# Kernel optimization log

Hardware: AMD Instinct MI355X
Metric: run time of the kernel (lower is better)

## Reference

```python
import jax, jax.numpy as jnp
import numpy as np

B, S, D = 4, 2048, 1024

def setup_inputs() -> dict:
    key = jax.random.key(0)
    ks = jax.random.split(key, 7)
    s = 1.0 / np.sqrt(D)
    return {
        "x":  jax.random.normal(ks[0], (B, S, D), dtype=jnp.float32),
        "Wq": jax.random.uniform(ks[1], (D, D), jnp.float32, -s, s),
        "bq": jax.random.uniform(ks[2], (D,),  jnp.float32, -s, s),
        "Wk": jax.random.uniform(ks[3], (D, D), jnp.float32, -s, s),
        "bk": jax.random.uniform(ks[4], (D,),  jnp.float32, -s, s),
        "Wv": jax.random.uniform(ks[5], (D, D), jnp.float32, -s, s),
        "bv": jax.random.uniform(ks[6], (D,),  jnp.float32, -s, s),
    }

def reference(x, Wq, bq, Wk, bk, Wv, bv):
    # Q/K/V projections: [B,S,D]
    Q = jnp.einsum('bsd,de->bse', x, Wq) + bq
    K = jnp.einsum('bsd,de->bse', x, Wk) + bk
    V = jnp.einsum('bsd,de->bse', x, Wv) + bv
    scale = 1.0 / jnp.sqrt(jnp.asarray(K.shape[-1], K.dtype))
    scores = jnp.einsum('bqd,bkd->bqk', Q, K) * scale  # [B,S,S]
    weights = jax.nn.softmax(scores, axis=-1)
    return jnp.einsum('bqk,bkd->bqd', weights, V)
```

## Files before the change

kernel.cpp:

```cpp
#include <hip/hip_runtime.h>

typedef __attribute__((ext_vector_type(4))) float f32x4;
typedef __attribute__((ext_vector_type(8))) short bf16x8;

__device__ __forceinline__ float bf2f(unsigned short u) {
  union { unsigned int i; float f; } x; x.i = ((unsigned int)u) << 16; return x.f;
}
__device__ __forceinline__ unsigned short f2bf(float f) {
  union { float f; unsigned int i; } x; x.f = f;
  unsigned int r = (x.i + 0x7FFFu + ((x.i >> 16) & 1u)) >> 16;
  return (unsigned short)r;
}

#define BARX __builtin_amdgcn_s_barrier()
#define LGK0 asm volatile("s_waitcnt lgkmcnt(0)" ::: "memory")
#define GLD(gsrc, ldsoff)                                                        \
  __builtin_amdgcn_global_load_lds(                                              \
      (const __attribute__((address_space(1))) void*)(gsrc),                     \
      (__attribute__((address_space(3))) void*)&lds[ldsoff], 16, 0, 0)

__global__ __launch_bounds__(256) void cvt_f2b(const float* __restrict__ src,
                                               unsigned short* __restrict__ dst, long n4) {
  long i = (long)blockIdx.x * 256 + threadIdx.x;
  long stride = (long)gridDim.x * 256;
  for (; i < n4; i += stride) {
    float4 v = *(const float4*)&src[i * 4];
    ushort4 o;
    o.x = f2bf(v.x); o.y = f2bf(v.y); o.z = f2bf(v.z); o.w = f2bf(v.w);
    *(ushort4*)&dst[i * 4] = o;
  }
}

__global__ __launch_bounds__(256) void transpose_f2b(const float* __restrict__ src,
                                                     unsigned short* __restrict__ dst,
                                                     int rows, int cols) {
  __shared__ float t[32][33];
  int bx = blockIdx.x * 32, by = blockIdx.y * 32;
  int tx = threadIdx.x, ty = threadIdx.y;
#pragma unroll
  for (int k = 0; k < 4; ++k)
    t[ty + 8 * k][tx] = src[(long)(by + ty + 8 * k) * cols + bx + tx];
  __syncthreads();
#pragma unroll
  for (int k = 0; k < 4; ++k)
    dst[(long)(bx + ty + 8 * k) * rows + by + tx] = f2bf(t[tx][ty + 8 * k]);
}

__global__ __launch_bounds__(256) void transpose_v(const unsigned short* __restrict__ src,
                                                   unsigned short* __restrict__ dst) {
  __shared__ unsigned short t[32][33];
  const long sb = (long)blockIdx.z * 2048 * 3072;
  const long db = (long)blockIdx.z * 1024 * 2048;
  int bx = blockIdx.x * 32, by = blockIdx.y * 32;
  int tx = threadIdx.x, ty = threadIdx.y;
#pragma unroll
  for (int k = 0; k < 4; ++k)
    t[ty + 8 * k][tx] = src[sb + (long)(by + ty + 8 * k) * 3072 + bx + tx];
  __syncthreads();
#pragma unroll
  for (int k = 0; k < 4; ++k)
    dst[db + (long)(bx + ty + 8 * k) * 2048 + by + tx] = t[tx][ty + 8 * k];
}

template <int MODE>
__global__ __launch_bounds__(512, 2) void gemm2p(const unsigned short* __restrict__ Ap,
                                                 const unsigned short* __restrict__ Bp,
                                                 void* __restrict__ Cv,
                                                 const float* __restrict__ q_,
                                                 const float* __restrict__ k_,
                                                 const float* __restrict__ v_,
                                                 const float* __restrict__ invden,
                                                 int Kd, int lda, int ldb, int ldc, float scale,
                                                 long sA, long sB, long sC) {
  __shared__ unsigned short lds[73728];
  const int bz = blockIdx.z;
  Ap += (long)bz * sA; Bp += (long)bz * sB;
  const int tid = threadIdx.x;
  const int m0 = blockIdx.x * 128, n0 = blockIdx.y * 256;
  const int lane = tid & 63, wave = tid >> 6;
  const int wm = wave >> 2, wn = wave & 3;
  const int rr = tid >> 3;
  const int cSrc = ((tid & 7) ^ (rr & 7)) << 3;
  const int lc = lane & 15, lr = lane >> 4;
  const int x0 = (lc & 4) << 3;
  const int x1 = 32 ^ x0;
  const int klo = (lr << 3) ^ ((lc & 3) << 3);
  const int aoff = (wm * 64 + lc) * 64 + klo;
  const int boff = 8192 + (wn * 64 + lc) * 64 + klo;
  const int NT = Kd >> 6;

  const unsigned short* pA0 = Ap + (long)(m0 + rr) * lda + cSrc;
  const unsigned short* pA1 = pA0 + (long)64 * lda;
  const unsigned short* pB0 = Bp + (long)(n0 + rr) * ldb + cSrc;
  const unsigned short* pB1 = pB0 + (long)64 * ldb;
  const unsigned short* pB2 = pB0 + (long)128 * ldb;
  const unsigned short* pB3 = pB0 + (long)192 * ldb;
  const int dA0 = tid * 8, dA1 = 4096 + tid * 8;
  const int dB0 = 8192 + tid * 8, dB1 = 12288 + tid * 8;
  const int dB2 = 16384 + tid * 8, dB3 = 20480 + tid * 8;
#define STAGE6(so)                                                                \
  { GLD(pB0, (so) + dB0); GLD(pB1, (so) + dB1); GLD(pA0, (so) + dA0);             \
    GLD(pB2, (so) + dB2); GLD(pB3, (so) + dB3); GLD(pA1, (so) + dA1); }
#define ADV { pA0 += 64; pA1 += 64; pB0 += 64; pB1 += 64; pB2 += 64; pB3 += 64; }

  f32x4 acc[4][4] = {};

  STAGE6(0); ADV;
  STAGE6(24576); ADV;
  asm volatile("s_waitcnt vmcnt(6)" ::: "memory");
  BARX;

  int cur = 0;
  for (int t = 0; t < NT; ++t) {
    const int stg = (cur >= 1) ? cur - 1 : 2;
    const unsigned short* Lp = &lds[cur * 24576];
    const int so = stg * 24576;
    const bool pf = (t + 2 < NT);
    bf16x8 a0[2][2], a1[2][2], bb[2][2][2];
#pragma unroll
    for (int nh = 0; nh < 2; ++nh)
#pragma unroll
      for (int ni = 0; ni < 2; ++ni) {
        bb[nh][ni][0] = *(const bf16x8*)&Lp[boff + nh * 2048 + ni * 1024 + x0];
        bb[nh][ni][1] = *(const bf16x8*)&Lp[boff + nh * 2048 + ni * 1024 + x1];
      }
#pragma unroll
    for (int mi = 0; mi < 2; ++mi) {
      a0[mi][0] = *(const bf16x8*)&Lp[aoff + mi * 1024 + x0];
      a0[mi][1] = *(const bf16x8*)&Lp[aoff + mi * 1024 + x1];
    }
    if (pf) { GLD(pB0, so + dB0); GLD(pB1, so + dB1); GLD(pA0, so + dA0); }
    BARX; LGK0;
    __builtin_amdgcn_s_setprio(1);
#pragma unroll
    for (int mi = 0; mi < 2; ++mi)
#pragma unroll
      for (int nh = 0; nh < 2; ++nh)
#pragma unroll
        for (int ni = 0; ni < 2; ++ni)
#pragma unroll
          for (int x = 0; x < 2; ++x)
            acc[mi][nh * 2 + ni] = __builtin_amdgcn_mfma_f32_16x16x32_bf16(
                a0[mi][x], bb[nh][ni][x], acc[mi][nh * 2 + ni], 0, 0, 0);
    __builtin_amdgcn_s_setprio(0);
    BARX;
#pragma unroll
    for (int mi = 0; mi < 2; ++mi) {
      a1[mi][0] = *(const bf16x8*)&Lp[aoff + 2048 + mi * 1024 + x0];
      a1[mi][1] = *(const bf16x8*)&Lp[aoff + 2048 + mi * 1024 + x1];
    }
    if (pf) { GLD(pB2, so + dB2); GLD(pB3, so + dB3); GLD(pA1, so + dA1); }
    BARX; LGK0;
    __builtin_amdgcn_s_setprio(1);
#pragma unroll
    for (int mi = 0; mi < 2; ++mi)
#pragma unroll
      for (int nh = 0; nh < 2; ++nh)
#pragma unroll
        for (int ni = 0; ni < 2; ++ni)
#pragma unroll
          for (int x = 0; x < 2; ++x)
            acc[2 + mi][nh * 2 + ni] = __builtin_amdgcn_mfma_f32_16x16x32_bf16(
                a1[mi][x], bb[nh][ni][x], acc[2 + mi][nh * 2 + ni], 0, 0, 0);
    __builtin_amdgcn_s_setprio(0);
    if (pf) { asm volatile("s_waitcnt vmcnt(6)" ::: "memory"); }
    else    { asm volatile("s_waitcnt vmcnt(0)" ::: "memory"); }
    BARX;
    cur = (cur == 2) ? 0 : cur + 1;
    ADV;
  }
#undef STAGE6
#undef ADV

  const int r0 = m0 + wm * 64 + lr * 4;
  const int c0 = n0 + wn * 64 + lc;
  if (MODE == 2) {
    float* O = (float*)Cv + (long)bz * sC;
    const float* idn = invden + (long)bz * 2048;
#pragma unroll
    for (int j = 0; j < 4; ++j)
#pragma unroll
      for (int r = 0; r < 4; ++r) {
        const int row = r0 + j * 16 + r;
        const float iv = idn[row];
#pragma unroll
        for (int nh = 0; nh < 2; ++nh)
#pragma unroll
          for (int ni = 0; ni < 2; ++ni)
            O[(long)row * ldc + (c0 + nh * 32 + ni * 16)] = acc[j][nh * 2 + ni][r] * iv;
      }
  } else {
    unsigned short* C = (unsigned short*)Cv + (long)bz * sC;
#pragma unroll
    for (int nh = 0; nh < 2; ++nh)
#pragma unroll
      for (int ni = 0; ni < 2; ++ni) {
        const int col = c0 + nh * 32 + ni * 16;
        float bv = 0.0f;
        if (MODE == 0)
          bv = (col < 1024) ? q_[col] : ((col < 2048) ? k_[col - 1024] : v_[col - 2048]);
#pragma unroll
        for (int j = 0; j < 4; ++j)
#pragma unroll
          for (int r = 0; r < 4; ++r) {
            float val = acc[j][nh * 2 + ni][r];
            val = (MODE == 0) ? (val + bv) : __expf(val * scale);
            C[(long)(r0 + j * 16 + r) * ldc + col] = f2bf(val);
          }
      }
  }
}

__global__ __launch_bounds__(256) void rowsum_inv(const unsigned short* __restrict__ E,
                                                  float* __restrict__ invden) {
  const long row = blockIdx.x;
  const unsigned short* p = E + row * 2048;
  const int tid = threadIdx.x;
  const int lane = tid & 63, wave = tid >> 6;
  ushort4 h0 = *(const ushort4*)&p[tid * 8];
  ushort4 h1 = *(const ushort4*)&p[tid * 8 + 4];
  float s = bf2f(h0.x) + bf2f(h0.y) + bf2f(h0.z) + bf2f(h0.w) +
            bf2f(h1.x) + bf2f(h1.y) + bf2f(h1.z) + bf2f(h1.w);
#pragma unroll
  for (int o = 32; o >= 1; o >>= 1) s += __shfl_xor(s, o);
  __shared__ float ss[4];
  if (lane == 0) ss[wave] = s;
  __syncthreads();
  if (tid == 0) invden[row] = 1.0f / (ss[0] + ss[1] + ss[2] + ss[3]);
}

extern "C" void kernel_launch(void* const* d_in, const int* in_sizes, int n_in,
                              void* d_out, int out_size, void* d_ws, size_t ws_size,
                              hipStream_t stream) {
  const float* x  = (const float*)d_in[0];
  const float* Wq = (const float*)d_in[1];
  const float* bq = (const float*)d_in[2];
  const float* Wk = (const float*)d_in[3];
  const float* bk = (const float*)d_in[4];
  const float* Wv = (const float*)d_in[5];
  const float* bv = (const float*)d_in[6];
  float* out = (float*)d_out;

  const int Bb = 4, S = 2048, D = 1024;
  const long MS = (long)Bb * S;

  char* ws = (char*)d_ws;
  unsigned short* xb  = (unsigned short*)(ws);
  unsigned short* Wt  = (unsigned short*)(ws + (16L << 20));
  unsigned short* QKV = (unsigned short*)(ws + (22L << 20));
  unsigned short* Sc  = (unsigned short*)(ws + (70L << 20));
  unsigned short* VT  = xb;
  float* invden = (float*)(ws + (16L << 20));

  cvt_f2b<<<2048, 256, 0, stream>>>(x, xb, MS * D / 4);

  dim3 tb(32, 8);
  dim3 tg(D / 32, D / 32);
  transpose_f2b<<<tg, tb, 0, stream>>>(Wq, Wt, D, D);
  transpose_f2b<<<tg, tb, 0, stream>>>(Wk, Wt + 1024 * 1024, D, D);
  transpose_f2b<<<tg, tb, 0, stream>>>(Wv, Wt + 2 * 1024 * 1024, D, D);

  dim3 pgrid(MS / 128, 3072 / 256, 1);
  gemm2p<0><<<pgrid, 512, 0, stream>>>(xb, Wt, QKV, bq, bk, bv, nullptr,
                                       D, D, D, 3072, 1.0f, 0, 0, 0);

  dim3 vtg(D / 32, S / 32, Bb);
  transpose_v<<<vtg, tb, 0, stream>>>(QKV + 2048, VT);

  dim3 sgrid(S / 128, S / 256, Bb);
  gemm2p<1><<<sgrid, 512, 0, stream>>>(QKV, QKV + 1024, Sc, nullptr, nullptr, nullptr, nullptr,
                                       D, 3072, 3072, S, 1.0f / 32.0f,
                                       (long)S * 3072, (long)S * 3072, (long)S * S);

  rowsum_inv<<<MS, 256, 0, stream>>>(Sc, invden);

  dim3 ogrid(S / 128, D / 256, Bb);
  gemm2p<2><<<ogrid, 512, 0, stream>>>(Sc, VT, out, nullptr, nullptr, nullptr, invden,
                                       S, S, S, D, 1.0f,
                                       (long)S * S, (long)D * S, (long)S * D);
}
```

Measured before the change: 180.6 us.

## Switch GEMMs to 128x128 double-buffered tiles and fuse row-sum into PV GEMM

Measured after the change: 173.2 us. -4.1%, faster.

```diff
diff --git a/kernel.cpp b/kernel.cpp
--- a/kernel.cpp
+++ b/kernel.cpp
@@ -14,6 +14,7 @@
 
 #define BARX __builtin_amdgcn_s_barrier()
 #define LGK0 asm volatile("s_waitcnt lgkmcnt(0)" ::: "memory")
+#define VM0  asm volatile("s_waitcnt vmcnt(0)" ::: "memory")
 #define GLD(gsrc, ldsoff)                                                        \
   __builtin_amdgcn_global_load_lds(                                              \
       (const __attribute__((address_space(1))) void*)(gsrc),                     \
@@ -46,39 +47,47 @@
     dst[(long)(bx + ty + 8 * k) * rows + by + tx] = f2bf(t[tx][ty + 8 * k]);
 }
 
-__global__ __launch_bounds__(256) void transpose_v(const unsigned short* __restrict__ src,
+__global__ __launch_bounds__(512) void transpose_v(const unsigned short* __restrict__ src,
                                                    unsigned short* __restrict__ dst) {
-  __shared__ unsigned short t[32][33];
+  __shared__ unsigned short t[64][65];
   const long sb = (long)blockIdx.z * 2048 * 3072;
-  const long db = (long)blockIdx.z * 1024 * 2048;
-  int bx = blockIdx.x * 32, by = blockIdx.y * 32;
-  int tx = threadIdx.x, ty = threadIdx.y;
-#pragma unroll
-  for (int k = 0; k < 4; ++k)
-    t[ty + 8 * k][tx] = src[sb + (long)(by + ty + 8 * k) * 3072 + bx + tx];
+  const long db = (long)blockIdx.z * 1024 * 2064;
+  const int d0 = blockIdx.x * 64;
+  const int s0 = blockIdx.y * 64;
+  const int tx = threadIdx.x, ty = threadIdx.y;
+#pragma unroll
+  for (int k = 0; k < 8; ++k)
+    t[ty + 8 * k][tx] = src[sb + (long)(s0 + ty + 8 * k) * 3072 + d0 + tx];
   __syncthreads();
 #pragma unroll
-  for (int k = 0; k < 4; ++k)
-    dst[db + (long)(bx + ty + 8 * k) * 2048 + by + tx] = t[tx][ty + 8 * k];
+  for (int k = 0; k < 8; ++k)
+    dst[db + (long)(d0 + ty + 8 * k) * 2064 + s0 + tx] = t[tx][ty + 8 * k];
 }
 
 template <int MODE>
-__global__ __launch_bounds__(512, 2) void gemm2p(const unsigned short* __restrict__ Ap,
-                                                 const unsigned short* __restrict__ Bp,
-                                                 void* __restrict__ Cv,
-                                                 const float* __restrict__ q_,
-                                                 const float* __restrict__ k_,
-                                                 const float* __restrict__ v_,
-                                                 const float* __restrict__ invden,
-                                                 int Kd, int lda, int ldb, int ldc, float scale,
-                                                 long sA, long sB, long sC) {
-  __shared__ unsigned short lds[73728];
-  const int bz = blockIdx.z;
-  Ap += (long)bz * sA; Bp += (long)bz * sB;
+__global__ __launch_bounds__(256, 2) void gemms(const unsigned short* __restrict__ Ap_,
+                                                const unsigned short* __restrict__ Bp_,
+                                                void* __restrict__ Cv,
+                                                const float* __restrict__ q_,
+                                                const float* __restrict__ k_,
+                                                const float* __restrict__ v_,
+                                                int Kd, int lda, int ldb, int ldc, float scale,
+                                                long sA, long sB, long sC) {
+  __shared__ unsigned short lds[32768];
+  int bx, by, bz;
+  if (MODE == 2) {
+    const int flat = blockIdx.x;
+    const int nid = ((flat & 7) << 6) | (flat >> 3);
+    bx = nid & 15; by = (nid >> 4) & 7; bz = nid >> 7;
+  } else {
+    bx = blockIdx.x; by = blockIdx.y; bz = blockIdx.z;
+  }
+  const unsigned short* Ap = Ap_ + (long)bz * sA;
+  const unsigned short* Bp = Bp_ + (long)bz * sB;
   const int tid = threadIdx.x;
-  const int m0 = blockIdx.x * 128, n0 = blockIdx.y * 256;
+  const int m0 = bx * 128, n0 = by * 128;
   const int lane = tid & 63, wave = tid >> 6;
-  const int wm = wave >> 2, wn = wave & 3;
+  const int wm = wave >> 1, wn = wave & 1;
   const int rr = tid >> 3;
   const int cSrc = ((tid & 7) ^ (rr & 7)) << 3;
   const int lc = lane & 15, lr = lane >> 4;
@@ -88,60 +97,54 @@
   const int aoff = (wm * 64 + lc) * 64 + klo;
   const int boff = 8192 + (wn * 64 + lc) * 64 + klo;
   const int NT = Kd >> 6;
-
-  const unsigned short* pA0 = Ap + (long)(m0 + rr) * lda + cSrc;
-  const unsigned short* pA1 = pA0 + (long)64 * lda;
-  const unsigned short* pB0 = Bp + (long)(n0 + rr) * ldb + cSrc;
-  const unsigned short* pB1 = pB0 + (long)64 * ldb;
-  const unsigned short* pB2 = pB0 + (long)128 * ldb;
-  const unsigned short* pB3 = pB0 + (long)192 * ldb;
-  const int dA0 = tid * 8, dA1 = 4096 + tid * 8;
-  const int dB0 = 8192 + tid * 8, dB1 = 12288 + tid * 8;
-  const int dB2 = 16384 + tid * 8, dB3 = 20480 + tid * 8;
-#define STAGE6(so)                                                                \
-  { GLD(pB0, (so) + dB0); GLD(pB1, (so) + dB1); GLD(pA0, (so) + dA0);             \
-    GLD(pB2, (so) + dB2); GLD(pB3, (so) + dB3); GLD(pA1, (so) + dA1); }
-#define ADV { pA0 += 64; pA1 += 64; pB0 += 64; pB1 += 64; pB2 += 64; pB3 += 64; }
+  const int rS = tid >> 1;
+  const int g0 = (tid & 1) * 4;
+
+  const unsigned short* pA = Ap + (long)(m0 + rr) * lda + cSrc;
+  const unsigned short* pB = Bp + (long)(n0 + rr) * ldb + cSrc;
+  const long a32 = (long)32 * lda, b32 = (long)32 * ldb;
+#define STA(so)                                                                   \
+  { GLD(pA, (so) + tid * 8);            GLD(pA + a32, (so) + 2048 + tid * 8);     \
+    GLD(pA + 2 * a32, (so) + 4096 + tid * 8); GLD(pA + 3 * a32, (so) + 6144 + tid * 8); }
+#define STB(so)                                                                   \
+  { GLD(pB, (so) + 8192 + tid * 8);     GLD(pB + b32, (so) + 10240 + tid * 8);    \
+    GLD(pB + 2 * b32, (so) + 12288 + tid * 8); GLD(pB + 3 * b32, (so) + 14336 + tid * 8); }
 
   f32x4 acc[4][4] = {};
-
-  STAGE6(0); ADV;
-  STAGE6(24576); ADV;
-  asm volatile("s_waitcnt vmcnt(6)" ::: "memory");
+  float esum = 0.0f;
+
+  STA(0); STB(0);
+  pA += 64; pB += 64;
+  VM0;
   BARX;
 
-  int cur = 0;
   for (int t = 0; t < NT; ++t) {
-    const int stg = (cur >= 1) ? cur - 1 : 2;
-    const unsigned short* Lp = &lds[cur * 24576];
-    const int so = stg * 24576;
-    const bool pf = (t + 2 < NT);
-    bf16x8 a0[2][2], a1[2][2], bb[2][2][2];
-#pragma unroll
-    for (int nh = 0; nh < 2; ++nh)
-#pragma unroll
-      for (int ni = 0; ni < 2; ++ni) {
-        bb[nh][ni][0] = *(const bf16x8*)&Lp[boff + nh * 2048 + ni * 1024 + x0];
-        bb[nh][ni][1] = *(const bf16x8*)&Lp[boff + nh * 2048 + ni * 1024 + x1];
-      }
+    const int p = t & 1;
+    const int soq = (p ^ 1) << 14;
+    const unsigned short* Lp = &lds[p << 14];
+    const bool pf = (t + 1 < NT);
+    bf16x8 a0[2][2], a1[2][2], bb[4][2];
+#pragma unroll
+    for (int ni = 0; ni < 4; ++ni) {
+      bb[ni][0] = *(const bf16x8*)&Lp[boff + ni * 1024 + x0];
+      bb[ni][1] = *(const bf16x8*)&Lp[boff + ni * 1024 + x1];
+    }
 #pragma unroll
     for (int mi = 0; mi < 2; ++mi) {
       a0[mi][0] = *(const bf16x8*)&Lp[aoff + mi * 1024 + x0];
       a0[mi][1] = *(const bf16x8*)&Lp[aoff + mi * 1024 + x1];
     }
-    if (pf) { GLD(pB0, so + dB0); GLD(pB1, so + dB1); GLD(pA0, so + dA0); }
+    if (pf) STA(soq);
     BARX; LGK0;
     __builtin_amdgcn_s_setprio(1);
 #pragma unroll
     for (int mi = 0; mi < 2; ++mi)
 #pragma unroll
-      for (int nh = 0; nh < 2; ++nh)
-#pragma unroll
-        for (int ni = 0; ni < 2; ++ni)
-#pragma unroll
-          for (int x = 0; x < 2; ++x)
-            acc[mi][nh * 2 + ni] = __builtin_amdgcn_mfma_f32_16x16x32_bf16(
-                a0[mi][x], bb[nh][ni][x], acc[mi][nh * 2 + ni], 0, 0, 0);
+      for (int ni = 0; ni < 4; ++ni)
+#pragma unroll
+        for (int x = 0; x < 2; ++x)
+          acc[mi][ni] = __builtin_amdgcn_mfma_f32_16x16x32_bf16(
+              a0[mi][x], bb[ni][x], acc[mi][ni], 0, 0, 0);
     __builtin_amdgcn_s_setprio(0);
     BARX;
 #pragma unroll
@@ -149,84 +152,69 @@
       a1[mi][0] = *(const bf16x8*)&Lp[aoff + 2048 + mi * 1024 + x0];
       a1[mi][1] = *(const bf16x8*)&Lp[aoff + 2048 + mi * 1024 + x1];
     }
-    if (pf) { GLD(pB2, so + dB2); GLD(pB3, so + dB3); GLD(pA1, so + dA1); }
+    if (MODE == 2) {
+#pragma unroll
+      for (int j = 0; j < 4; ++j) {
+        bf16x8 s = *(const bf16x8*)&Lp[rS * 64 + (((g0 + j) ^ (rS & 7)) << 3)];
+#pragma unroll
+        for (int e = 0; e < 8; ++e) esum += bf2f((unsigned short)s[e]);
+      }
+    }
+    if (pf) STB(soq);
     BARX; LGK0;
     __builtin_amdgcn_s_setprio(1);
 #pragma unroll
     for (int mi = 0; mi < 2; ++mi)
 #pragma unroll
-      for (int nh = 0; nh < 2; ++nh)
-#pragma unroll
-        for (int ni = 0; ni < 2; ++ni)
-#pragma unroll
-          for (int x = 0; x < 2; ++x)
-            acc[2 + mi][nh * 2 + ni] = __builtin_amdgcn_mfma_f32_16x16x32_bf16(
-                a1[mi][x], bb[nh][ni][x], acc[2 + mi][nh * 2 + ni], 0, 0, 0);
+      for (int ni = 0; ni < 4; ++ni)
+#pragma unroll
+        for (int x = 0; x < 2; ++x)
+          acc[2 + mi][ni] = __builtin_amdgcn_mfma_f32_16x16x32_bf16(
+              a1[mi][x], bb[ni][x], acc[2 + mi][ni], 0, 0, 0);
     __builtin_amdgcn_s_setprio(0);
-    if (pf) { asm volatile("s_waitcnt vmcnt(6)" ::: "memory"); }
-    else    { asm volatile("s_waitcnt vmcnt(0)" ::: "memory"); }
+    VM0;
     BARX;
-    cur = (cur == 2) ? 0 : cur + 1;
-    ADV;
-  }
-#undef STAGE6
-#undef ADV
+    pA += 64; pB += 64;
+  }
+#undef STA
+#undef STB
 
   const int r0 = m0 + wm * 64 + lr * 4;
   const int c0 = n0 + wn * 64 + lc;
   if (MODE == 2) {
+    esum += __shfl_xor(esum, 1);
+    float* sums = (float*)lds;
+    if ((tid & 1) == 0) sums[tid >> 1] = esum;
+    __syncthreads();
     float* O = (float*)Cv + (long)bz * sC;
-    const float* idn = invden + (long)bz * 2048;
-#pragma unroll
-    for (int j = 0; j < 4; ++j)
+#pragma unroll
+    for (int mi = 0; mi < 4; ++mi)
 #pragma unroll
       for (int r = 0; r < 4; ++r) {
-        const int row = r0 + j * 16 + r;
-        const float iv = idn[row];
-#pragma unroll
-        for (int nh = 0; nh < 2; ++nh)
-#pragma unroll
-          for (int ni = 0; ni < 2; ++ni)
-            O[(long)row * ldc + (c0 + nh * 32 + ni * 16)] = acc[j][nh * 2 + ni][r] * iv;
+        const int l = wm * 64 + mi * 16 + lr * 4 + r;
+        const float iv = 1.0f / sums[l];
+#pragma unroll
+        for (int ni = 0; ni < 4; ++ni)
+          O[(long)(m0 + l) * ldc + (c0 + ni * 16)] = acc[mi][ni][r] * iv;
       }
   } else {
     unsigned short* C = (unsigned short*)Cv + (long)bz * sC;
 #pragma unroll
-    for (int nh = 0; nh < 2; ++nh)
-#pragma unroll
-      for (int ni = 0; ni < 2; ++ni) {
-        const int col = c0 + nh * 32 + ni * 16;
-        float bv = 0.0f;
-        if (MODE == 0)
-          bv = (col < 1024) ? q_[col] : ((col < 2048) ? k_[col - 1024] : v_[col - 2048]);
-#pragma unroll
-        for (int j = 0; j < 4; ++j)
-#pragma unroll
-          for (int r = 0; r < 4; ++r) {
-            float val = acc[j][nh * 2 + ni][r];
-            val = (MODE == 0) ? (val + bv) : __expf(val * scale);
-            C[(long)(r0 + j * 16 + r) * ldc + col] = f2bf(val);
-          }
-      }
-  }
-}
-
-__global__ __launch_bounds__(256) void rowsum_inv(const unsigned short* __restrict__ E,
-                                                  float* __restrict__ invden) {
-  const long row = blockIdx.x;
-  const unsigned short* p = E + row * 2048;
-  const int tid = threadIdx.x;
-  const int lane = tid & 63, wave = tid >> 6;
-  ushort4 h0 = *(const ushort4*)&p[tid * 8];
-  ushort4 h1 = *(const ushort4*)&p[tid * 8 + 4];
-  float s = bf2f(h0.x) + bf2f(h0.y) + bf2f(h0.z) + bf2f(h0.w) +
-            bf2f(h1.x) + bf2f(h1.y) + bf2f(h1.z) + bf2f(h1.w);
-#pragma unroll
-  for (int o = 32; o >= 1; o >>= 1) s += __shfl_xor(s, o);
-  __shared__ float ss[4];
-  if (lane == 0) ss[wave] = s;
-  __syncthreads();
-  if (tid == 0) invden[row] = 1.0f / (ss[0] + ss[1] + ss[2] + ss[3]);
+    for (int ni = 0; ni < 4; ++ni) {
+      const int col = c0 + ni * 16;
+      float bv = 0.0f;
+      if (MODE == 0)
+        bv = (col < 1024) ? q_[col] : ((col < 2048) ? k_[col - 1024] : v_[col - 2048]);
+#pragma unroll
+      for (int mi = 0; mi < 4; ++mi)
+#pragma unroll
+        for (int r = 0; r < 4; ++r) {
+          float val = acc[mi][ni][r];
+          val = (MODE == 0) ? (val + bv) : __expf(val * scale);
+          C[(long)(r0 + mi * 16 + r) * ldc + col] = f2bf(val);
+        }
+    }
+  }
 }
 
 extern "C" void kernel_launch(void* const* d_in, const int* in_sizes, int n_in,
@@ -243,6 +231,7 @@
 
   const int Bb = 4, S = 2048, D = 1024;
   const long MS = (long)Bb * S;
+  const int LDP = 2064;
 
   char* ws = (char*)d_ws;
   unsigned short* xb  = (unsigned short*)(ws);
@@ -250,7 +239,6 @@
   unsigned short* QKV = (unsigned short*)(ws + (22L << 20));
   unsigned short* Sc  = (unsigned short*)(ws + (70L << 20));
   unsigned short* VT  = xb;
-  float* invden = (float*)(ws + (16L << 20));
 
   cvt_f2b<<<2048, 256, 0, stream>>>(x, xb, MS * D / 4);
 
@@ -260,22 +248,20 @@
   transpose_f2b<<<tg, tb, 0, stream>>>(Wk, Wt + 1024 * 1024, D, D);
   transpose_f2b<<<tg, tb, 0, stream>>>(Wv, Wt + 2 * 1024 * 1024, D, D);
 
-  dim3 pgrid(MS / 128, 3072 / 256, 1);
-  gemm2p<0><<<pgrid, 512, 0, stream>>>(xb, Wt, QKV, bq, bk, bv, nullptr,
-                                       D, D, D, 3072, 1.0f, 0, 0, 0);
-
-  dim3 vtg(D / 32, S / 32, Bb);
-  transpose_v<<<vtg, tb, 0, stream>>>(QKV + 2048, VT);
-
-  dim3 sgrid(S / 128, S / 256, Bb);
-  gemm2p<1><<<sgrid, 512, 0, stream>>>(QKV, QKV + 1024, Sc, nullptr, nullptr, nullptr, nullptr,
-                                       D, 3072, 3072, S, 1.0f / 32.0f,
-                                       (long)S * 3072, (long)S * 3072, (long)S * S);
-
-  rowsum_inv<<<MS, 256, 0, stream>>>(Sc, invden);
-
-  dim3 ogrid(S / 128, D / 256, Bb);
-  gemm2p<2><<<ogrid, 512, 0, stream>>>(Sc, VT, out, nullptr, nullptr, nullptr, invden,
-                                       S, S, S, D, 1.0f,
-                                       (long)S * S, (long)D * S, (long)S * D);
-}
+  dim3 pgrid(MS / 128, 3072 / 128, 1);
+  gemms<0><<<pgrid, 256, 0, stream>>>(xb, Wt, QKV, bq, bk, bv,
+                                      D, D, D, 3072, 1.0f, 0, 0, 0);
+
+  dim3 vtb(64, 8);
+  dim3 vtg(D / 64, S / 64, Bb);
+  transpose_v<<<vtg, vtb, 0, stream>>>(QKV + 2048, VT);
+
+  dim3 sgrid(S / 128, S / 128, Bb);
+  gemms<1><<<sgrid, 256, 0, stream>>>(QKV, QKV + 1024, Sc, nullptr, nullptr, nullptr,
+                                      D, 3072, 3072, LDP, 1.0f / 32.0f,
+                                      (long)S * 3072, (long)S * 3072, (long)S * LDP);
+
+  gemms<2><<<512, 256, 0, stream>>>(Sc, VT, out, nullptr, nullptr, nullptr,
+                                    2048, LDP, LDP, D, 1.0f,
+                                    (long)S * LDP, (long)D * LDP, (long)S * D);
+}
```
